# Kernel optimization log

Measured on AMD Instinct MI355X. Metric: run time of the kernel, lower is better.

Reference implementation:

```python
import math
import jax, jax.numpy as jnp
import numpy as np

B, T, E = 2, 2048, 1024
H, KV = 16, 4
D = E // H          # 64
G = H // KV         # 4 groups


def rotate_half(x):
    x1, x2 = jnp.split(x, 2, axis=-1)
    return jnp.concatenate([-x2, x1], axis=-1)


def setup_inputs() -> dict:
    key = jax.random.key(0)
    ks = jax.random.split(key, 12)
    query = jax.random.normal(ks[0], (B, T, E), jnp.float32)
    key_t = jax.random.normal(ks[1], (B, T, E), jnp.float32)
    value = jax.random.normal(ks[2], (B, T, E), jnp.float32)
    # RoPE tables: [T, D]
    inv_freq = 1.0 / (10000.0 ** (np.arange(0, D, 2, dtype=np.float32) / D))
    pos = np.arange(T, dtype=np.float32)
    freqs = np.outer(pos, inv_freq)                      # [T, D/2]
    emb = np.concatenate([freqs, freqs], axis=-1)        # [T, D]
    cos_emb = jnp.asarray(np.cos(emb), jnp.float32)
    sin_emb = jnp.asarray(np.sin(emb), jnp.float32)
    # causal mask [1,1,T,T], True = keep
    mask = jnp.tril(jnp.ones((T, T), bool))[None, None, :, :]
    s = 0.02
    Wq = jax.random.normal(ks[3], (E, H * D), jnp.float32) * s
    bq = jnp.zeros((H * D,), jnp.float32)
    Wk = jax.random.normal(ks[4], (E, KV * D), jnp.float32) * s
    bk = jnp.zeros((KV * D,), jnp.float32)
    Wv = jax.random.normal(ks[5], (E, KV * D), jnp.float32) * s
    bv = jnp.zeros((KV * D,), jnp.float32)
    Wo = jax.random.normal(ks[6], (E, E), jnp.float32) * s
    bo = jnp.zeros((E,), jnp.float32)
    return {"query": query, "key": key_t, "value": value,
            "cos_emb": cos_emb, "sin_emb": sin_emb, "mask": mask,
            "Wq": Wq, "bq": bq, "Wk": Wk, "bk": bk,
            "Wv": Wv, "bv": bv, "Wo": Wo, "bo": bo}


def reference(query, key, value, cos_emb, sin_emb, mask,
              Wq, bq, Wk, bk, Wv, bv, Wo, bo):
    Bq, Tq, _ = query.shape
    Tk = key.shape[1]
    q = (query @ Wq + bq).reshape(Bq, Tq, H, D)          # [B,Tq,H,D]
    k = (key @ Wk + bk).reshape(Bq, Tk, KV, D)           # [B,Tk,KV,D]
    v = (value @ Wv + bv).reshape(Bq, Tk, KV, D)
    # expand kv heads across groups (head h = kv*G + g, consecutive repeat)
    k = jnp.repeat(k, G, axis=2)                         # [B,Tk,H,D]
    v = jnp.repeat(v, G, axis=2)
    # RoPE (applied post-expansion, as in the original)
    cos = cos_emb[None, :, None, :]                      # [1,T,1,D]
    sin = sin_emb[None, :, None, :]
    q = q * cos[:, :Tq] + rotate_half(q) * sin[:, :Tq]
    k = k * cos[:, :Tk] + rotate_half(k) * sin[:, :Tk]
    scores = jnp.einsum('bqhd,bkhd->bhqk', q, k) / math.sqrt(D)
    scores = jnp.where(mask[:, :, :Tq, :Tk], scores, jnp.float32(-jnp.inf))
    probs = jax.nn.softmax(scores, axis=-1)              # [B,H,Tq,Tk]
    attn = jnp.einsum('bhqk,bkhd->bqhd', probs, v).reshape(Bq, Tq, E)
    return attn @ Wo + bo
```

## Files before the change

kernel.cpp:

```cpp
#include <hip/hip_runtime.h>
#include <hip/hip_bf16.h>

constexpr int Bc  = 2;
constexpr int Tc  = 2048;
constexpr int Ec  = 1024;
constexpr int Hc  = 16;
constexpr int KVc = 4;
constexpr int Dc  = 64;

typedef short bf16x8 __attribute__((ext_vector_type(8)));
typedef short short4v __attribute__((ext_vector_type(4)));
typedef float f32x4  __attribute__((ext_vector_type(4)));
typedef float f32x16 __attribute__((ext_vector_type(16)));
typedef int   i32x4  __attribute__((ext_vector_type(4)));

__device__ inline short f2bf_bits(float f) {
    union { __hip_bfloat16 h; short s; } u;
    u.h = __float2bfloat16(f);
    return u.s;
}

__device__ inline float bf2f(short s) {
    union { short s16; __hip_bfloat16 h; } u;
    u.s16 = s;
    return __bfloat162float(u.h);
}

__device__ inline unsigned pkbf(float a, float b) {
    union { __hip_bfloat162 h2; unsigned u; } u;
    u.h2 = __float22bfloat162_rn(float2{a, b});
    return u.u;
}

__device__ inline float fexp2(float x) { return __builtin_exp2f(x); }

__device__ inline void permswap(unsigned &a, unsigned &b) {
    asm volatile("v_permlane32_swap_b32 %0, %1" : "+v"(a), "+v"(b));
}

__device__ inline void gload16(const short* g, short* lds) {
    __builtin_amdgcn_global_load_lds(
        (const __attribute__((address_space(1))) unsigned int*)g,
        (__attribute__((address_space(3))) unsigned int*)lds,
        16, 0, 0);
}

__global__ __launch_bounds__(256) void conv3_f32_bf16(
    const float* __restrict__ q, const float* __restrict__ k,
    const float* __restrict__ v,
    short* __restrict__ Xq, short* __restrict__ Xk, short* __restrict__ Xv)
{
    const int range = blockIdx.x >> 12;
    const int sub   = blockIdx.x & 4095;
    const float* x = range == 0 ? q : (range == 1 ? k : v);
    short*       y = range == 0 ? Xq : (range == 1 ? Xk : Xv);
    int i = (sub * 256 + threadIdx.x) * 4;
    float4 vv = *reinterpret_cast<const float4*>(x + i);
    short4v o;
    o[0] = f2bf_bits(vv.x);
    o[1] = f2bf_bits(vv.y);
    o[2] = f2bf_bits(vv.z);
    o[3] = f2bf_bits(vv.w);
    *reinterpret_cast<short4v*>(y + i) = o;
}

__global__ __launch_bounds__(256) void transp_all(
    const float* __restrict__ Wq, const float* __restrict__ Wk,
    const float* __restrict__ Wv, const float* __restrict__ Wo,
    short* __restrict__ Wqt, short* __restrict__ Wkt,
    short* __restrict__ Wvt, short* __restrict__ Wot)
{
    __shared__ float tile[32][33];
    const int id = blockIdx.x;
    const float* W; short* Wt; int N, bx, by;
    if (id < 1024)      { W = Wq; Wt = Wqt; N = 1024; bx = id & 31;          by = id >> 5; }
    else if (id < 1280) { W = Wk; Wt = Wkt; N = 256;  bx = (id - 1024) & 7;  by = (id - 1024) >> 3; }
    else if (id < 1536) { W = Wv; Wt = Wvt; N = 256;  bx = (id - 1280) & 7;  by = (id - 1280) >> 3; }
    else                { W = Wo; Wt = Wot; N = 1024; bx = (id - 1536) & 31; by = (id - 1536) >> 5; }
    const int K = 1024;
    int nb = bx * 32, kb = by * 32;
    int tx = threadIdx.x & 31, ty = threadIdx.x >> 5;
    #pragma unroll
    for (int j = 0; j < 4; ++j)
        tile[ty + j * 8][tx] = W[(size_t)(kb + ty + j * 8) * N + nb + tx];
    __syncthreads();
    #pragma unroll
    for (int j = 0; j < 4; ++j)
        Wt[(size_t)(nb + ty + j * 8) * K + kb + tx] = f2bf_bits(tile[tx][ty + j * 8]);
}

#define GEMM_CORE(A_, Bt_, Kdim_)                                              \
    const int lane = threadIdx.x & 63;                                         \
    const int w    = threadIdx.x >> 6;                                         \
    const int wm   = w >> 1, wn = w & 1;                                       \
    const int rin  = lane >> 3;                                                \
    const int swc  = ((lane & 7) ^ rin) * 8;                                   \
    f32x4 acc[4][2] = {};                                                      \
    for (int k0 = 0; k0 < (Kdim_); k0 += 64) {                                 \
        _Pragma("unroll")                                                      \
        for (int i2 = 0; i2 < 4; ++i2) {                                       \
            const int r = w * 32 + i2 * 8;                                     \
            gload16((A_) + (size_t)(m0 + r + rin) * (Kdim_) + k0 + swc,        \
                    As + r * 64);                                              \
        }                                                                      \
        _Pragma("unroll")                                                      \
        for (int i2 = 0; i2 < 2; ++i2) {                                       \
            const int r = w * 16 + i2 * 8;                                     \
            gload16((Bt_) + (size_t)(n0 + r + rin) * (Kdim_) + k0 + swc,       \
                    Bs + r * 64);                                              \
        }                                                                      \
        __syncthreads();                                                       \
        _Pragma("unroll")                                                      \
        for (int ks = 0; ks < 2; ++ks) {                                       \
            bf16x8 af[4], bfr[2];                                              \
            _Pragma("unroll")                                                  \
            for (int mi = 0; mi < 4; ++mi) {                                   \
                int row = wm * 64 + mi * 16 + (lane & 15);                     \
                int sl  = (ks * 4 + (lane >> 4)) ^ (row & 7);                  \
                af[mi] = *reinterpret_cast<const bf16x8*>(As + row * 64 + sl * 8); \
            }                                                                  \
            _Pragma("unroll")                                                  \
            for (int ni = 0; ni < 2; ++ni) {                                   \
                int row = wn * 32 + ni * 16 + (lane & 15);                     \
                int sl  = (ks * 4 + (lane >> 4)) ^ (row & 7);                  \
                bfr[ni] = *reinterpret_cast<const bf16x8*>(Bs + row * 64 + sl * 8); \
            }                                                                  \
            _Pragma("unroll")                                                  \
            for (int mi = 0; mi < 4; ++mi)                                     \
                _Pragma("unroll")                                              \
                for (int ni = 0; ni < 2; ++ni)                                 \
                    acc[mi][ni] = __builtin_amdgcn_mfma_f32_16x16x32_bf16(     \
                        af[mi], bfr[ni], acc[mi][ni], 0, 0, 0);                \
        }                                                                      \
        __syncthreads();                                                       \
    }

__global__ __launch_bounds__(256) void gemm_qkv(
    const short* __restrict__ Xq, const short* __restrict__ Xk,
    const short* __restrict__ Xv,
    const short* __restrict__ Wqt, const short* __restrict__ Wkt,
    const short* __restrict__ Wvt,
    const float* __restrict__ bq, const float* __restrict__ bk,
    const float* __restrict__ bv,
    const float* __restrict__ cosE, const float* __restrict__ sinE,
    short* __restrict__ Qp, short* __restrict__ Kp, short* __restrict__ VTp)
{
    __shared__ short As[128 * 64];
    __shared__ short Bs[64 * 64];
    const int gid = blockIdx.x;
    const short *A, *Bt; const float* bias; int bx, by, mode;
    if (gid < 512)      { mode = 0; A = Xq; Bt = Wqt; bias = bq; bx = gid & 15;         by = gid >> 4; }
    else if (gid < 640) { mode = 1; A = Xk; Bt = Wkt; bias = bk; bx = (gid - 512) & 3;  by = (gid - 512) >> 2; }
    else                { mode = 2; A = Xv; Bt = Wvt; bias = bv; bx = (gid - 640) & 3;  by = (gid - 640) >> 2; }
    const int m0 = by * 128, n0 = bx * 64;

    GEMM_CORE(A, Bt, 1024)

    if (mode == 2) {
        #pragma unroll
        for (int mi = 0; mi < 4; ++mi)
            #pragma unroll
            for (int ni = 0; ni < 2; ++ni) {
                int col = n0 + wn * 32 + ni * 16 + (lane & 15);
                float bv2 = bias[col];
                #pragma unroll
                for (int i = 0; i < 4; ++i) {
                    int row = m0 + wm * 64 + mi * 16 + ((lane >> 4) * 4) + i;
                    VTp[(((size_t)(row >> 11) * 256 + col) << 11) + (row & 2047)]
                        = f2bf_bits(acc[mi][ni][i] + bv2);
                }
            }
        return;
    }

    #pragma unroll
    for (int mi = 0; mi < 4; ++mi)
        #pragma unroll
        for (int ni = 0; ni < 2; ++ni) {
            int cl = wn * 32 + ni * 16 + (lane & 15);
            float bv2 = bias[n0 + cl];
            #pragma unroll
            for (int i = 0; i < 4; ++i) {
                int rl = wm * 64 + mi * 16 + ((lane >> 4) * 4) + i;
                As[rl * 64 + cl] = f2bf_bits(acc[mi][ni][i] + bv2);
            }
        }
    __syncthreads();

    const float scale = (mode == 0) ? 0.125f * 1.44269504089f : 1.0f;
    short* outp = (mode == 0) ? Qp : Kp;
    const int ldo = (mode == 0) ? 1024 : 256;
    const int dg  = (threadIdx.x & 7) * 4;
    const int rb  = threadIdx.x >> 3;
    #pragma unroll
    for (int rr = 0; rr < 4; ++rr) {
        int rl = rb + rr * 32;
        int t  = (m0 + rl) & (Tc - 1);
        float4 c4 = *reinterpret_cast<const float4*>(cosE + t * 64 + dg);
        float4 s4 = *reinterpret_cast<const float4*>(sinE + t * 64 + dg);
        short4v a = *reinterpret_cast<const short4v*>(As + rl * 64 + dg);
        short4v b = *reinterpret_cast<const short4v*>(As + rl * 64 + 32 + dg);
        float c[4] = {c4.x, c4.y, c4.z, c4.w};
        float s[4] = {s4.x, s4.y, s4.z, s4.w};
        short4v oa, ob;
        #pragma unroll
        for (int j = 0; j < 4; ++j) {
            float x1 = bf2f(a[j]), x2 = bf2f(b[j]);
            oa[j] = f2bf_bits((x1 * c[j] - x2 * s[j]) * scale);
            ob[j] = f2bf_bits((x2 * c[j] + x1 * s[j]) * scale);
        }
        size_t go = (size_t)(m0 + rl) * ldo + n0 + dg;
        *reinterpret_cast<short4v*>(outp + go)      = oa;
        *reinterpret_cast<short4v*>(outp + go + 32) = ob;
    }
}

__global__ __launch_bounds__(256) void gemm_o(
    const short* __restrict__ A, const short* __restrict__ Bt,
    const float* __restrict__ bias, float* __restrict__ C)
{
    __shared__ short As[128 * 64];
    __shared__ short Bs[64 * 64];
    const int m0 = blockIdx.y * 128, n0 = blockIdx.x * 64;

    GEMM_CORE(A, Bt, 1024)

    #pragma unroll
    for (int mi = 0; mi < 4; ++mi)
        #pragma unroll
        for (int ni = 0; ni < 2; ++ni) {
            int col = n0 + wn * 32 + ni * 16 + (lane & 15);
            float bv2 = bias[col];
            #pragma unroll
            for (int i = 0; i < 4; ++i) {
                int row = m0 + wm * 64 + mi * 16 + ((lane >> 4) * 4) + i;
                C[(size_t)row * 1024 + col] = acc[mi][ni][i] + bv2;
            }
        }
}

__global__ __launch_bounds__(256, 4) void flash_gqa10(
    const short* __restrict__ Q,
    const short* __restrict__ Kx,
    const short* __restrict__ VT,
    short* __restrict__ attn,
    short* __restrict__ PO,
    float* __restrict__ ML)
{
    __shared__ short smem[16384];

    const int lane = threadIdx.x & 63;
    const int w    = threadIdx.x >> 6;
    const int lo   = lane & 31;
    const int hi   = lane >> 5;

    const int L   = blockIdx.x;
    const int xcd = L & 7;
    const int j   = L >> 3;
    const int g   = j & 3;
    const int u   = 39 - (j >> 2);
    int qt = 0, rem = u;
    while (true) { int nc0 = (qt >> 2) + 1; if (rem < nc0) break; rem -= nc0; ++qt; }
    const int c  = rem;
    const int nc = (qt >> 2) + 1;
    const int b   = xcd >> 2;
    const int kvh = xcd & 3;
    const int h   = kvh * 4 + g;
    const int slot = (b * 16 + h) * 40 + u;

    const int q0w = qt * 128 + w * 32;
    const int qg  = q0w + lo;

    bf16x8 qf[4];
    {
        const short* qp = Q + (size_t)(b * Tc + qg) * Ec + h * 64 + hi * 8;
        #pragma unroll
        for (int ds = 0; ds < 4; ++ds)
            qf[ds] = *reinterpret_cast<const bf16x8*>(qp + 16 * ds);
    }
    const short* Kb = Kx + (size_t)b * Tc * (KVc * Dc) + kvh * 64;
    const short* Vb = VT + (size_t)(b * KVc + kvh) * 64 * Tc;

    const int rin = lane >> 3;
    const int swc = ((lane & 7) ^ rin) * 8;
    auto stage = [&](int bufi, int kb2) {
        #pragma unroll
        for (int i2 = 0; i2 < 2; ++i2) {
            const int row = w * 16 + i2 * 8;
            gload16(Kb + (size_t)(kb2 + row + rin) * 256 + swc,
                    smem + bufi * 4096 + row * 64);
            gload16(Vb + (size_t)(row + rin) * Tc + kb2 + swc,
                    smem + 8192 + bufi * 4096 + row * 64);
        }
    };

    int slot8[4];
    #pragma unroll
    for (int i = 0; i < 4; ++i)
        slot8[i] = (((2 * i + hi) ^ (lo & 7)) * 8) + lo * 64;

    const int t0 = c * 8;
    const int t1 = min(c * 8 + 8, 2 * qt + 2);
    stage(0, t0 * 64);

    float m = -1e30f, l = 0.f;
    f32x16 o0 = {}, o1 = {};
    const int kv_hi = q0w + 32;

    for (int t = t0; t < t1; ++t) {
        const int kb  = t * 64;
        const int cur = (t - t0) & 1;
        asm volatile("s_waitcnt vmcnt(0)" ::: "memory");
        __builtin_amdgcn_s_barrier();
        if (t + 1 < t1) stage(cur ^ 1, kb + 64);

        if (kb < kv_hi) {
            const short* Kl = smem + cur * 4096;
            const short* Vl = Kl + 8192;

            f32x16 s0 = {}, s1 = {};
            __builtin_amdgcn_s_setprio(1);
            #pragma unroll
            for (int ds = 0; ds < 4; ++ds) {
                bf16x8 k0 = *reinterpret_cast<const bf16x8*>(Kl + slot8[ds]);
                bf16x8 k1 = *reinterpret_cast<const bf16x8*>(Kl + slot8[ds] + 2048);
                s0 = __builtin_amdgcn_mfma_f32_32x32x16_bf16(k0, qf[ds], s0, 0, 0, 0);
                s1 = __builtin_amdgcn_mfma_f32_32x32x16_bf16(k1, qf[ds], s1, 0, 0, 0);
            }
            __builtin_amdgcn_s_setprio(0);

            if (kb + 63 > q0w) {
                #pragma unroll
                for (int r = 0; r < 16; ++r) {
                    int kkl = (r & 3) + 8 * (r >> 2) + 4 * hi;
                    if (kb + kkl > qg)      s0[r] = -1e30f;
                    if (kb + 32 + kkl > qg) s1[r] = -1e30f;
                }
            }

            float mx[8];
            #pragma unroll
            for (int j2 = 0; j2 < 8; ++j2)
                mx[j2] = fmaxf(fmaxf(s0[2 * j2], s0[2 * j2 + 1]),
                               fmaxf(s1[2 * j2], s1[2 * j2 + 1]));
            #pragma unroll
            for (int st = 4; st > 0; st >>= 1)
                #pragma unroll
                for (int j2 = 0; j2 < st; ++j2) mx[j2] = fmaxf(mx[j2], mx[j2 + st]);
            float pm = fmaxf(mx[0], __shfl_xor(mx[0], 32));

            float corr = 1.0f;
            if (__any(pm > m + 8.0f)) {
                float mn = fmaxf(m, pm);
                corr = fexp2(m - mn);
                m = mn;
                #pragma unroll
                for (int r = 0; r < 16; ++r) { o0[r] *= corr; o1[r] *= corr; }
            }
            float rs = 0.f;
            #pragma unroll
            for (int r = 0; r < 16; ++r) {
                s0[r] = fexp2(s0[r] - m);
                s1[r] = fexp2(s1[r] - m);
                rs += s0[r] + s1[r];
            }
            rs += __shfl_xor(rs, 32);
            l = l * corr + rs;

            #pragma unroll
            for (int t2 = 0; t2 < 2; ++t2) {
                const f32x16& sv = t2 ? s1 : s0;
                unsigned pw[8];
                #pragma unroll
                for (int j2 = 0; j2 < 8; ++j2)
                    pw[j2] = pkbf(sv[2 * j2], sv[2 * j2 + 1]);
                #pragma unroll
                for (int u2 = 0; u2 < 2; ++u2) {
                    permswap(pw[4 * u2 + 0], pw[4 * u2 + 2]);
                    permswap(pw[4 * u2 + 1], pw[4 * u2 + 3]);
                    union { unsigned u4[4]; bf16x8 v; } pf;
                    pf.u4[0] = pw[4 * u2 + 0];
                    pf.u4[1] = pw[4 * u2 + 1];
                    pf.u4[2] = pw[4 * u2 + 2];
                    pf.u4[3] = pw[4 * u2 + 3];
                    int sl = 2 * t2 + u2;
                    bf16x8 v0 = *reinterpret_cast<const bf16x8*>(Vl + slot8[sl]);
                    bf16x8 v1 = *reinterpret_cast<const bf16x8*>(Vl + slot8[sl] + 2048);
                    __builtin_amdgcn_s_setprio(1);
                    o0 = __builtin_amdgcn_mfma_f32_32x32x16_bf16(v0, pf.v, o0, 0, 0, 0);
                    o1 = __builtin_amdgcn_mfma_f32_32x32x16_bf16(v1, pf.v, o1, 0, 0, 0);
                    __builtin_amdgcn_s_setprio(0);
                }
            }
        }
    }
    __builtin_amdgcn_s_barrier();

    const float inv = (nc == 1) ? (1.0f / l) : 1.0f;
    short* ob = smem + w * 2048;
    #pragma unroll
    for (int r = 0; r < 16; ++r) {
        int d0 = (r & 3) + 8 * (r >> 2) + 4 * hi;
        ob[lo * 64 + ( d0       ^ ((lo & 7) << 3))] = f2bf_bits(o0[r] * inv);
        ob[lo * 64 + ((d0 + 32) ^ ((lo & 7) << 3))] = f2bf_bits(o1[r] * inv);
    }
    if (nc > 1 && hi == 0) {
        ML[(size_t)slot * 256 + (w * 32 + lo) * 2]     = m;
        ML[(size_t)slot * 256 + (w * 32 + lo) * 2 + 1] = l;
    }
    #pragma unroll
    for (int j2 = 0; j2 < 4; ++j2) {
        int row = lane >> 1;
        int c8  = ((lane & 1) * 4 + j2) * 8;
        bf16x8 v = *reinterpret_cast<const bf16x8*>(
            ob + row * 64 + (c8 ^ ((row & 7) << 3)));
        if (nc == 1)
            *reinterpret_cast<bf16x8*>(
                attn + (size_t)(b * Tc + q0w + row) * Ec + h * 64 + c8) = v;
        else
            *reinterpret_cast<bf16x8*>(
                PO + (size_t)slot * 8192 + (w * 32 + row) * 64 + c8) = v;
    }
}

__global__ __launch_bounds__(256) void combine_kernel(
    const short* __restrict__ PO, const float* __restrict__ ML,
    short* __restrict__ attn)
{
    const int qt    = 4 + (blockIdx.x >> 2);
    const int rg    = blockIdx.x & 3;
    const int combo = blockIdx.y;
    const int h = combo & 15, b = combo >> 4;
    const int nc = (qt >> 2) + 1;
    const int k  = qt >> 2, r4 = qt & 3;
    const int base = (k + 1) * (2 * k + r4);
    const int slot0 = combo * 40 + base;

    const int r  = rg * 32 + (threadIdx.x >> 3);
    const int d8 = (threadIdx.x & 7) * 8;

    float mv[4], lv[4];
    float M = -1e30f;
    #pragma unroll 4
    for (int cc = 0; cc < nc; ++cc) {
        mv[cc] = ML[(size_t)(slot0 + cc) * 256 + r * 2];
        lv[cc] = ML[(size_t)(slot0 + cc) * 256 + r * 2 + 1];
        M = fmaxf(M, mv[cc]);
    }
    float Lsum = 0.f;
    float a[8] = {};
    #pragma unroll 4
    for (int cc = 0; cc < nc; ++cc) {
        float wgt = fexp2(mv[cc] - M);
        Lsum += wgt * lv[cc];
        bf16x8 po = *reinterpret_cast<const bf16x8*>(
            PO + (size_t)(slot0 + cc) * 8192 + r * 64 + d8);
        #pragma unroll
        for (int j = 0; j < 8; ++j) a[j] += wgt * bf2f(po[j]);
    }
    float inv = 1.0f / Lsum;
    bf16x8 o;
    #pragma unroll
    for (int j = 0; j < 8; ++j) o[j] = f2bf_bits(a[j] * inv);
    *reinterpret_cast<bf16x8*>(
        attn + (size_t)(b * Tc + qt * 128 + r) * Ec + h * 64 + d8) = o;
}

extern "C" void kernel_launch(void* const* d_in, const int* in_sizes, int n_in,
                              void* d_out, int out_size, void* d_ws, size_t ws_size,
                              hipStream_t stream)
{
    const float* query = (const float*)d_in[0];
    const float* key   = (const float*)d_in[1];
    const float* value = (const float*)d_in[2];
    const float* cosE  = (const float*)d_in[3];
    const float* sinE  = (const float*)d_in[4];
    const float* Wq = (const float*)d_in[6];
    const float* bq = (const float*)d_in[7];
    const float* Wk = (const float*)d_in[8];
    const float* bk = (const float*)d_in[9];
    const float* Wv = (const float*)d_in[10];
    const float* bv = (const float*)d_in[11];
    const float* Wo = (const float*)d_in[12];
    const float* bo = (const float*)d_in[13];

    char* ws = (char*)d_ws;
    constexpr size_t MB = 1u << 20;
    short* Xq   = (short*)(ws + 0);
    short* Xk   = (short*)(ws + 8  * MB);
    short* Xv   = (short*)(ws + 16 * MB);
    short* Wqt  = (short*)(ws + 24 * MB);
    short* Wkt  = (short*)(ws + 26 * MB);
    short* Wvt  = (short*)(ws + 26 * MB + 512 * 1024);
    short* Wot  = (short*)(ws + 27 * MB);
    short* Qp   = (short*)(ws + 29 * MB);
    short* Kp   = (short*)(ws + 37 * MB);
    short* VTp  = (short*)(ws + 39 * MB);
    short* attn = (short*)(ws + 41 * MB);
    short* PO   = (short*)(ws + 0);
    float* ML   = (float*)(ws + 21 * MB);
    (void)ws_size;

    conv3_f32_bf16<<<12288, 256, 0, stream>>>(query, key, value, Xq, Xk, Xv);
    transp_all<<<2560, 256, 0, stream>>>(Wq, Wk, Wv, Wo, Wqt, Wkt, Wvt, Wot);
    gemm_qkv<<<768, 256, 0, stream>>>(Xq, Xk, Xv, Wqt, Wkt, Wvt,
                                      bq, bk, bv, cosE, sinE, Qp, Kp, VTp);
    flash_gqa10<<<1280, 256, 0, stream>>>(Qp, Kp, VTp, attn, PO, ML);
    combine_kernel<<<dim3(48, 32), 256, 0, stream>>>(PO, ML, attn);
    gemm_o<<<dim3(16, 32), 256, 0, stream>>>(attn, Wot, bo, (float*)d_out);
}
```

Before: 111.8 us.

## Pre-pack K and V into MFMA fragment order and load directly to registers

The QKV projection kernel now writes K and V tiles in a packed layout that matches the per-lane MFMA fragment order, going through a swizzled LDS staging buffer. The attention kernel drops its LDS double-buffered staging and barriers. Each wave loads K/V fragments straight from global memory into registers, with contiguous 16-byte loads per lane. The loop also stops at the causal bound per wave rather than per block. The trade-off is no LDS sharing of K/V across the four waves, so more global/L2 traffic, and load latency is now hidden only by occupancy and the compiler's scheduling.

```diff
diff --git a/kernel.cpp b/kernel.cpp
--- a/kernel.cpp
+++ b/kernel.cpp
@@ -143,7 +143,7 @@
     const float* __restrict__ bq, const float* __restrict__ bk,
     const float* __restrict__ bv,
     const float* __restrict__ cosE, const float* __restrict__ sinE,
-    short* __restrict__ Qp, short* __restrict__ Kp, short* __restrict__ VTp)
+    short* __restrict__ Qp, short* __restrict__ Kpack, short* __restrict__ Vpack)
 {
     __shared__ short As[128 * 64];
     __shared__ short Bs[64 * 64];
@@ -156,22 +156,7 @@
 
     GEMM_CORE(A, Bt, 1024)
 
-    if (mode == 2) {
-        #pragma unroll
-        for (int mi = 0; mi < 4; ++mi)
-            #pragma unroll
-            for (int ni = 0; ni < 2; ++ni) {
-                int col = n0 + wn * 32 + ni * 16 + (lane & 15);
-                float bv2 = bias[col];
-                #pragma unroll
-                for (int i = 0; i < 4; ++i) {
-                    int row = m0 + wm * 64 + mi * 16 + ((lane >> 4) * 4) + i;
-                    VTp[(((size_t)(row >> 11) * 256 + col) << 11) + (row & 2047)]
-                        = f2bf_bits(acc[mi][ni][i] + bv2);
-                }
-            }
-        return;
-    }
+    const int lo = lane & 31, hi = lane >> 5;
 
     #pragma unroll
     for (int mi = 0; mi < 4; ++mi)
@@ -182,14 +167,31 @@
             #pragma unroll
             for (int i = 0; i < 4; ++i) {
                 int rl = wm * 64 + mi * 16 + ((lane >> 4) * 4) + i;
-                As[rl * 64 + cl] = f2bf_bits(acc[mi][ni][i] + bv2);
+                As[rl * 64 + (cl ^ ((rl & 7) << 3))] = f2bf_bits(acc[mi][ni][i] + bv2);
             }
         }
     __syncthreads();
 
+    if (mode == 2) {
+        const int bq2  = m0 >> 11;
+        const int tb   = (m0 & 2047) >> 6;
+        const int sub  = w >> 1, td = w & 1;
+        size_t vbase = (((size_t)(bq2 * 4 + bx) * 32 + tb + sub) * 4096)
+                     + (size_t)td * 2048;
+        #pragma unroll
+        for (int sl = 0; sl < 4; ++sl) {
+            union { short s[8]; bf16x8 v; } vw;
+            #pragma unroll
+            for (int j2 = 0; j2 < 8; ++j2) {
+                int row = sub * 64 + 16 * sl + 8 * hi + j2;
+                vw.s[j2] = As[row * 64 + ((32 * td + lo) ^ (j2 << 3))];
+            }
+            *reinterpret_cast<bf16x8*>(Vpack + vbase + sl * 512 + lane * 8) = vw.v;
+        }
+        return;
+    }
+
     const float scale = (mode == 0) ? 0.125f * 1.44269504089f : 1.0f;
-    short* outp = (mode == 0) ? Qp : Kp;
-    const int ldo = (mode == 0) ? 1024 : 256;
     const int dg  = (threadIdx.x & 7) * 4;
     const int rb  = threadIdx.x >> 3;
     #pragma unroll
@@ -198,20 +200,42 @@
         int t  = (m0 + rl) & (Tc - 1);
         float4 c4 = *reinterpret_cast<const float4*>(cosE + t * 64 + dg);
         float4 s4 = *reinterpret_cast<const float4*>(sinE + t * 64 + dg);
-        short4v a = *reinterpret_cast<const short4v*>(As + rl * 64 + dg);
-        short4v b = *reinterpret_cast<const short4v*>(As + rl * 64 + 32 + dg);
+        int sa = rl * 64 + (dg ^ ((rl & 7) << 3));
+        int sb = rl * 64 + ((dg + 32) ^ ((rl & 7) << 3));
+        short4v a = *reinterpret_cast<const short4v*>(As + sa);
+        short4v b = *reinterpret_cast<const short4v*>(As + sb);
         float c[4] = {c4.x, c4.y, c4.z, c4.w};
         float s[4] = {s4.x, s4.y, s4.z, s4.w};
         short4v oa, ob;
         #pragma unroll
-        for (int j = 0; j < 4; ++j) {
-            float x1 = bf2f(a[j]), x2 = bf2f(b[j]);
-            oa[j] = f2bf_bits((x1 * c[j] - x2 * s[j]) * scale);
-            ob[j] = f2bf_bits((x2 * c[j] + x1 * s[j]) * scale);
-        }
-        size_t go = (size_t)(m0 + rl) * ldo + n0 + dg;
-        *reinterpret_cast<short4v*>(outp + go)      = oa;
-        *reinterpret_cast<short4v*>(outp + go + 32) = ob;
+        for (int j2 = 0; j2 < 4; ++j2) {
+            float x1 = bf2f(a[j2]), x2 = bf2f(b[j2]);
+            oa[j2] = f2bf_bits((x1 * c[j2] - x2 * s[j2]) * scale);
+            ob[j2] = f2bf_bits((x2 * c[j2] + x1 * s[j2]) * scale);
+        }
+        if (mode == 0) {
+            size_t go = (size_t)(m0 + rl) * 1024 + n0 + dg;
+            *reinterpret_cast<short4v*>(Qp + go)      = oa;
+            *reinterpret_cast<short4v*>(Qp + go + 32) = ob;
+        } else {
+            *reinterpret_cast<short4v*>(As + sa) = oa;
+            *reinterpret_cast<short4v*>(As + sb) = ob;
+        }
+    }
+    if (mode == 0) return;
+
+    __syncthreads();
+    const int bq2 = m0 >> 11;
+    const int tb  = (m0 & 2047) >> 6;
+    const int sub = w >> 1, t2 = w & 1;
+    const int row = sub * 64 + 32 * t2 + lo;
+    size_t kbase = (((size_t)(bq2 * 4 + bx) * 32 + tb + sub) * 4096)
+                 + (size_t)t2 * 2048;
+    #pragma unroll
+    for (int ds = 0; ds < 4; ++ds) {
+        bf16x8 v = *reinterpret_cast<const bf16x8*>(
+            As + row * 64 + ((16 * ds + 8 * hi) ^ ((row & 7) << 3)));
+        *reinterpret_cast<bf16x8*>(Kpack + kbase + ds * 512 + lane * 8) = v;
     }
 }
 
@@ -239,15 +263,15 @@
         }
 }
 
-__global__ __launch_bounds__(256, 4) void flash_gqa10(
+__global__ __launch_bounds__(256, 4) void flash_gqa12(
     const short* __restrict__ Q,
-    const short* __restrict__ Kx,
-    const short* __restrict__ VT,
+    const short* __restrict__ Kpack,
+    const short* __restrict__ Vpack,
     short* __restrict__ attn,
     short* __restrict__ PO,
     float* __restrict__ ML)
 {
-    __shared__ short smem[16384];
+    __shared__ short obuf[4 * 2048];
 
     const int lane = threadIdx.x & 63;
     const int w    = threadIdx.x >> 6;
@@ -278,126 +302,108 @@
         for (int ds = 0; ds < 4; ++ds)
             qf[ds] = *reinterpret_cast<const bf16x8*>(qp + 16 * ds);
     }
-    const short* Kb = Kx + (size_t)b * Tc * (KVc * Dc) + kvh * 64;
-    const short* Vb = VT + (size_t)(b * KVc + kvh) * 64 * Tc;
-
-    const int rin = lane >> 3;
-    const int swc = ((lane & 7) ^ rin) * 8;
-    auto stage = [&](int bufi, int kb2) {
-        #pragma unroll
-        for (int i2 = 0; i2 < 2; ++i2) {
-            const int row = w * 16 + i2 * 8;
-            gload16(Kb + (size_t)(kb2 + row + rin) * 256 + swc,
-                    smem + bufi * 4096 + row * 64);
-            gload16(Vb + (size_t)(row + rin) * Tc + kb2 + swc,
-                    smem + 8192 + bufi * 4096 + row * 64);
-        }
-    };
-
-    int slot8[4];
-    #pragma unroll
-    for (int i = 0; i < 4; ++i)
-        slot8[i] = (((2 * i + hi) ^ (lo & 7)) * 8) + lo * 64;
+    const short* Kb = Kpack + (size_t)(b * KVc + kvh) * 32 * 4096;
+    const short* Vb = Vpack + (size_t)(b * KVc + kvh) * 32 * 4096;
+    const int woff = lane * 8;
 
     const int t0 = c * 8;
     const int t1 = min(c * 8 + 8, 2 * qt + 2);
-    stage(0, t0 * 64);
+    const int te = min(t1, (q0w + 95) >> 6);
 
     float m = -1e30f, l = 0.f;
     f32x16 o0 = {}, o1 = {};
-    const int kv_hi = q0w + 32;
-
-    for (int t = t0; t < t1; ++t) {
-        const int kb  = t * 64;
-        const int cur = (t - t0) & 1;
-        asm volatile("s_waitcnt vmcnt(0)" ::: "memory");
-        __builtin_amdgcn_s_barrier();
-        if (t + 1 < t1) stage(cur ^ 1, kb + 64);
-
-        if (kb < kv_hi) {
-            const short* Kl = smem + cur * 4096;
-            const short* Vl = Kl + 8192;
-
-            f32x16 s0 = {}, s1 = {};
-            __builtin_amdgcn_s_setprio(1);
-            #pragma unroll
-            for (int ds = 0; ds < 4; ++ds) {
-                bf16x8 k0 = *reinterpret_cast<const bf16x8*>(Kl + slot8[ds]);
-                bf16x8 k1 = *reinterpret_cast<const bf16x8*>(Kl + slot8[ds] + 2048);
-                s0 = __builtin_amdgcn_mfma_f32_32x32x16_bf16(k0, qf[ds], s0, 0, 0, 0);
-                s1 = __builtin_amdgcn_mfma_f32_32x32x16_bf16(k1, qf[ds], s1, 0, 0, 0);
+
+    for (int t = t0; t < te; ++t) {
+        const int kb = t * 64;
+        const short* Kt = Kb + (size_t)t * 4096;
+        const short* Vt = Vb + (size_t)t * 4096;
+
+        bf16x8 vf0[4];
+        #pragma unroll
+        for (int sl = 0; sl < 4; ++sl)
+            vf0[sl] = *reinterpret_cast<const bf16x8*>(Vt + sl * 512 + woff);
+
+        f32x16 s0 = {}, s1 = {};
+        __builtin_amdgcn_s_setprio(1);
+        #pragma unroll
+        for (int ds = 0; ds < 4; ++ds) {
+            bf16x8 k0 = *reinterpret_cast<const bf16x8*>(Kt + ds * 512 + woff);
+            bf16x8 k1 = *reinterpret_cast<const bf16x8*>(Kt + 2048 + ds * 512 + woff);
+            s0 = __builtin_amdgcn_mfma_f32_32x32x16_bf16(k0, qf[ds], s0, 0, 0, 0);
+            s1 = __builtin_amdgcn_mfma_f32_32x32x16_bf16(k1, qf[ds], s1, 0, 0, 0);
+        }
+        __builtin_amdgcn_s_setprio(0);
+
+        bf16x8 vf1[4];
+        #pragma unroll
+        for (int sl = 0; sl < 4; ++sl)
+            vf1[sl] = *reinterpret_cast<const bf16x8*>(Vt + 2048 + sl * 512 + woff);
+
+        if (kb + 63 > q0w) {
+            #pragma unroll
+            for (int r = 0; r < 16; ++r) {
+                int kkl = (r & 3) + 8 * (r >> 2) + 4 * hi;
+                if (kb + kkl > qg)      s0[r] = -1e30f;
+                if (kb + 32 + kkl > qg) s1[r] = -1e30f;
             }
-            __builtin_amdgcn_s_setprio(0);
-
-            if (kb + 63 > q0w) {
-                #pragma unroll
-                for (int r = 0; r < 16; ++r) {
-                    int kkl = (r & 3) + 8 * (r >> 2) + 4 * hi;
-                    if (kb + kkl > qg)      s0[r] = -1e30f;
-                    if (kb + 32 + kkl > qg) s1[r] = -1e30f;
-                }
+        }
+
+        float mx[8];
+        #pragma unroll
+        for (int j2 = 0; j2 < 8; ++j2)
+            mx[j2] = fmaxf(fmaxf(s0[2 * j2], s0[2 * j2 + 1]),
+                           fmaxf(s1[2 * j2], s1[2 * j2 + 1]));
+        #pragma unroll
+        for (int st = 4; st > 0; st >>= 1)
+            #pragma unroll
+            for (int j2 = 0; j2 < st; ++j2) mx[j2] = fmaxf(mx[j2], mx[j2 + st]);
+        float pm = fmaxf(mx[0], __shfl_xor(mx[0], 32));
+
+        float corr = 1.0f;
+        if (__any(pm > m + 8.0f)) {
+            float mn = fmaxf(m, pm);
+            corr = fexp2(m - mn);
+            m = mn;
+            #pragma unroll
+            for (int r = 0; r < 16; ++r) { o0[r] *= corr; o1[r] *= corr; }
+        }
+        float rs = 0.f;
+        #pragma unroll
+        for (int r = 0; r < 16; ++r) {
+            s0[r] = fexp2(s0[r] - m);
+            s1[r] = fexp2(s1[r] - m);
+            rs += s0[r] + s1[r];
+        }
+        rs += __shfl_xor(rs, 32);
+        l = l * corr + rs;
+
+        #pragma unroll
+        for (int t2 = 0; t2 < 2; ++t2) {
+            const f32x16& sv = t2 ? s1 : s0;
+            unsigned pw[8];
+            #pragma unroll
+            for (int j2 = 0; j2 < 8; ++j2)
+                pw[j2] = pkbf(sv[2 * j2], sv[2 * j2 + 1]);
+            #pragma unroll
+            for (int u2 = 0; u2 < 2; ++u2) {
+                permswap(pw[4 * u2 + 0], pw[4 * u2 + 2]);
+                permswap(pw[4 * u2 + 1], pw[4 * u2 + 3]);
+                union { unsigned u4[4]; bf16x8 v; } pf;
+                pf.u4[0] = pw[4 * u2 + 0];
+                pf.u4[1] = pw[4 * u2 + 1];
+                pf.u4[2] = pw[4 * u2 + 2];
+                pf.u4[3] = pw[4 * u2 + 3];
+                int sl = 2 * t2 + u2;
+                __builtin_amdgcn_s_setprio(1);
+                o0 = __builtin_amdgcn_mfma_f32_32x32x16_bf16(vf0[sl], pf.v, o0, 0, 0, 0);
+                o1 = __builtin_amdgcn_mfma_f32_32x32x16_bf16(vf1[sl], pf.v, o1, 0, 0, 0);
+                __builtin_amdgcn_s_setprio(0);
             }
-
-            float mx[8];
-            #pragma unroll
-            for (int j2 = 0; j2 < 8; ++j2)
-                mx[j2] = fmaxf(fmaxf(s0[2 * j2], s0[2 * j2 + 1]),
-                               fmaxf(s1[2 * j2], s1[2 * j2 + 1]));
-            #pragma unroll
-            for (int st = 4; st > 0; st >>= 1)
-                #pragma unroll
-                for (int j2 = 0; j2 < st; ++j2) mx[j2] = fmaxf(mx[j2], mx[j2 + st]);
-            float pm = fmaxf(mx[0], __shfl_xor(mx[0], 32));
-
-            float corr = 1.0f;
-            if (__any(pm > m + 8.0f)) {
-                float mn = fmaxf(m, pm);
-                corr = fexp2(m - mn);
-                m = mn;
-                #pragma unroll
-                for (int r = 0; r < 16; ++r) { o0[r] *= corr; o1[r] *= corr; }
-            }
-            float rs = 0.f;
-            #pragma unroll
-            for (int r = 0; r < 16; ++r) {
-                s0[r] = fexp2(s0[r] - m);
-                s1[r] = fexp2(s1[r] - m);
-                rs += s0[r] + s1[r];
-            }
-            rs += __shfl_xor(rs, 32);
-            l = l * corr + rs;
-
-            #pragma unroll
-            for (int t2 = 0; t2 < 2; ++t2) {
-                const f32x16& sv = t2 ? s1 : s0;
-                unsigned pw[8];
-                #pragma unroll
-                for (int j2 = 0; j2 < 8; ++j2)
-                    pw[j2] = pkbf(sv[2 * j2], sv[2 * j2 + 1]);
-                #pragma unroll
-                for (int u2 = 0; u2 < 2; ++u2) {
-                    permswap(pw[4 * u2 + 0], pw[4 * u2 + 2]);
-                    permswap(pw[4 * u2 + 1], pw[4 * u2 + 3]);
-                    union { unsigned u4[4]; bf16x8 v; } pf;
-                    pf.u4[0] = pw[4 * u2 + 0];
-                    pf.u4[1] = pw[4 * u2 + 1];
-                    pf.u4[2] = pw[4 * u2 + 2];
-                    pf.u4[3] = pw[4 * u2 + 3];
-                    int sl = 2 * t2 + u2;
-                    bf16x8 v0 = *reinterpret_cast<const bf16x8*>(Vl + slot8[sl]);
-                    bf16x8 v1 = *reinterpret_cast<const bf16x8*>(Vl + slot8[sl] + 2048);
-                    __builtin_amdgcn_s_setprio(1);
-                    o0 = __builtin_amdgcn_mfma_f32_32x32x16_bf16(v0, pf.v, o0, 0, 0, 0);
-                    o1 = __builtin_amdgcn_mfma_f32_32x32x16_bf16(v1, pf.v, o1, 0, 0, 0);
-                    __builtin_amdgcn_s_setprio(0);
-                }
-            }
-        }
-    }
-    __builtin_amdgcn_s_barrier();
+        }
+    }
 
     const float inv = (nc == 1) ? (1.0f / l) : 1.0f;
-    short* ob = smem + w * 2048;
+    short* ob = obuf + w * 2048;
     #pragma unroll
     for (int r = 0; r < 16; ++r) {
         int d0 = (r & 3) + 8 * (r >> 2) + 4 * hi;
@@ -486,26 +492,26 @@
 
     char* ws = (char*)d_ws;
     constexpr size_t MB = 1u << 20;
-    short* Xq   = (short*)(ws + 0);
-    short* Xk   = (short*)(ws + 8  * MB);
-    short* Xv   = (short*)(ws + 16 * MB);
-    short* Wqt  = (short*)(ws + 24 * MB);
-    short* Wkt  = (short*)(ws + 26 * MB);
-    short* Wvt  = (short*)(ws + 26 * MB + 512 * 1024);
-    short* Wot  = (short*)(ws + 27 * MB);
-    short* Qp   = (short*)(ws + 29 * MB);
-    short* Kp   = (short*)(ws + 37 * MB);
-    short* VTp  = (short*)(ws + 39 * MB);
-    short* attn = (short*)(ws + 41 * MB);
-    short* PO   = (short*)(ws + 0);
-    float* ML   = (float*)(ws + 21 * MB);
+    short* Xq    = (short*)(ws + 0);
+    short* Xk    = (short*)(ws + 8  * MB);
+    short* Xv    = (short*)(ws + 16 * MB);
+    short* Wqt   = (short*)(ws + 24 * MB);
+    short* Wkt   = (short*)(ws + 26 * MB);
+    short* Wvt   = (short*)(ws + 26 * MB + 512 * 1024);
+    short* Wot   = (short*)(ws + 27 * MB);
+    short* Qp    = (short*)(ws + 29 * MB);
+    short* Kpack = (short*)(ws + 37 * MB);
+    short* Vpack = (short*)(ws + 39 * MB);
+    short* attn  = (short*)(ws + 41 * MB);
+    short* PO    = (short*)(ws + 0);
+    float* ML    = (float*)(ws + 21 * MB);
     (void)ws_size;
 
     conv3_f32_bf16<<<12288, 256, 0, stream>>>(query, key, value, Xq, Xk, Xv);
     transp_all<<<2560, 256, 0, stream>>>(Wq, Wk, Wv, Wo, Wqt, Wkt, Wvt, Wot);
     gemm_qkv<<<768, 256, 0, stream>>>(Xq, Xk, Xv, Wqt, Wkt, Wvt,
-                                      bq, bk, bv, cosE, sinE, Qp, Kp, VTp);
-    flash_gqa10<<<1280, 256, 0, stream>>>(Qp, Kp, VTp, attn, PO, ML);
+                                      bq, bk, bv, cosE, sinE, Qp, Kpack, Vpack);
+    flash_gqa12<<<1280, 256, 0, stream>>>(Qp, Kpack, Vpack, attn, PO, ML);
     combine_kernel<<<dim3(48, 32), 256, 0, stream>>>(PO, ML, attn);
     gemm_o<<<dim3(16, 32), 256, 0, stream>>>(attn, Wot, bo, (float*)d_out);
 }
```

After: 118.7 us. 6.2% more time.
